# Optimization experiments

Measured on AMD Instinct MI355X. Metric: run time of the kernel, lower is better.

The kernel has to match this reference:

```python
import jax, jax.numpy as jnp
import numpy as np

N, E = 40000, 640000
IN_DIM, EDGE_DIM, HID, H1 = 5, 11, 128, 4
NEG_SLOPE = 0.2


def _add_self_loops(ei, ea, n):
    # PyG GATConv default: add_self_loops=True, fill_value='mean' for edge_attr
    loop = jnp.arange(n, dtype=ei.dtype)
    ei2 = jnp.concatenate([ei, jnp.stack([loop, loop])], axis=1)
    ea2 = jnp.concatenate([ea, jnp.broadcast_to(ea.mean(0), (n, ea.shape[1]))], axis=0)
    return ei2, ea2


def _gat(x, ei, ea, W, We, a_src, a_dst, a_edge, b, H, C):
    # Single GATConv layer (eval mode, dropout inactive)
    n = x.shape[0]
    xh = (x @ W).reshape(n, H, C)            # [N,H,C]
    eh = (ea @ We).reshape(-1, H, C)         # [E,H,C]
    src, dst = ei[0], ei[1]
    a_s = (xh * a_src).sum(-1)               # [N,H]
    a_d = (xh * a_dst).sum(-1)               # [N,H]
    alpha = jax.nn.leaky_relu(a_s[src] + a_d[dst] + (eh * a_edge).sum(-1), NEG_SLOPE)  # [E,H]
    amax = jax.ops.segment_max(alpha, dst, num_segments=n)
    ex = jnp.exp(alpha - amax[dst])
    den = jax.ops.segment_sum(ex, dst, num_segments=n)
    w = ex / (den[dst] + 1e-16)              # softmax over inbound edges per dst
    out = jax.ops.segment_sum(xh[src] * w[:, :, None], dst, num_segments=n)  # [N,H,C]
    return out.reshape(n, H * C) + b


def setup_inputs() -> dict:
    key = jax.random.key(0)
    ks = jax.random.split(key, 20)
    s = 0.1
    return {
        "x": jax.random.normal(ks[0], (N, IN_DIM), jnp.float32),
        "edge_index": jax.random.randint(ks[1], (2, E), 0, N),
        "edge_attr": jax.random.normal(ks[2], (E, EDGE_DIM), jnp.float32),
        "W1": jax.random.normal(ks[3], (IN_DIM, H1 * HID), jnp.float32) * s,
        "We1": jax.random.normal(ks[4], (EDGE_DIM, H1 * HID), jnp.float32) * s,
        "a_src1": jax.random.normal(ks[5], (H1, HID), jnp.float32) * s,
        "a_dst1": jax.random.normal(ks[6], (H1, HID), jnp.float32) * s,
        "a_edge1": jax.random.normal(ks[7], (H1, HID), jnp.float32) * s,
        "b1": jnp.zeros((H1 * HID,), jnp.float32),
        # layer 2 (512 -> 128, 1 head)
        "W2": jax.random.normal(ks[8], (H1 * HID, HID), jnp.float32) * s,
        "We2": jax.random.normal(ks[9], (EDGE_DIM, HID), jnp.float32) * s,
        "a_src2": jax.random.normal(ks[10], (1, HID), jnp.float32) * s,
        "a_dst2": jax.random.normal(ks[11], (1, HID), jnp.float32) * s,
        "a_edge2": jax.random.normal(ks[12], (1, HID), jnp.float32) * s,
        "b2": jnp.zeros((HID,), jnp.float32),
        # final linear 128 -> 1
        "Wfc": jax.random.normal(ks[13], (HID, 1), jnp.float32) * s,
        "bfc": jnp.zeros((1,), jnp.float32),
    }


def reference(x, edge_index, edge_attr,
              W1, We1, a_src1, a_dst1, a_edge1, b1,
              W2, We2, a_src2, a_dst2, a_edge2, b2,
              Wfc, bfc):
    ei, ea = _add_self_loops(edge_index, edge_attr, x.shape[0])
    h = jax.nn.relu(_gat(x, ei, ea, W1, We1, a_src1, a_dst1, a_edge1, b1, H1, HID))
    h = jax.nn.relu(_gat(h, ei, ea, W2, We2, a_src2, a_dst2, a_edge2, b2, 1, HID))
    return jax.nn.sigmoid(h @ Wfc + bfc)
```

## Files before the change

### kernel.cpp

```cpp
#include <hip/hip_runtime.h>

#define NN   40000
#define EE   640000
#define IND  5
#define ED   11
#define HIDD 128
#define F1   512
#define PSB  2500

typedef unsigned short u16;
typedef unsigned int   u32;
typedef __attribute__((ext_vector_type(8))) short bf16x8;
typedef __attribute__((ext_vector_type(4))) float f32x4;

__device__ __forceinline__ float bf2f(u16 u) { return __uint_as_float(((u32)u) << 16); }
__device__ __forceinline__ u16 f2bf(float f) {
    u32 u = __float_as_uint(f);
    return (u16)((u + 0x7FFFu + ((u >> 16) & 1u)) >> 16);
}

__device__ __forceinline__ float wsum(float v) {
#pragma unroll
    for (int o = 32; o; o >>= 1) v += __shfl_xor(v, o, 64);
    return v;
}
__device__ __forceinline__ float lrelu(float v) { return v > 0.f ? v : 0.2f * v; }


#define SBLK 256
#define SGRID ((NN + SBLK - 1) / SBLK)
#define PREPG (PSB + 33 + NN / 4)

__global__ void __launch_bounds__(256) k_prep(const int* __restrict__ ei,
                                              int* __restrict__ counts,
                                              int* __restrict__ rank,
                                              float* __restrict__ consts,
                                              const float* __restrict__ We1,
                                              const float* __restrict__ ae1,
                                              const float* __restrict__ We2,
                                              const float* __restrict__ ae2,
                                              const float* __restrict__ W2,
                                              u16* __restrict__ bsw,
                                              const float* __restrict__ x,
                                              const float* __restrict__ W1,
                                              const float* __restrict__ as1,
                                              const float* __restrict__ ad1,
                                              float* __restrict__ aS1,
                                              float* __restrict__ aD1) {
    int bid = blockIdx.x, t = threadIdx.x;
    if (bid < PSB) {
        int i = bid * 256 + t;
        rank[i] = atomicAdd(&counts[ei[EE + i]], 1);
        return;
    }
    if (bid == PSB) {
        if (t < 44) {
            int k = t >> 2, h = t & 3;
            float s = 0.f;
            for (int c = 0; c < HIDD; ++c)
                s += We1[k * F1 + h * HIDD + c] * ae1[h * HIDD + c];
            consts[16 + t] = s;
        }
        if (t >= 48 && t < 48 + ED) {
            int k = t - 48;
            float s = 0.f;
            for (int c = 0; c < HIDD; ++c)
                s += We2[k * HIDD + c] * ae2[c];
            consts[64 + k] = s;
        }
        return;
    }
    if (bid < PSB + 33) {
        int t2 = (bid - (PSB + 1)) * 256 + t;
        if (t2 >= 8192) return;
        int lane = t2 & 63, ks = (t2 >> 6) & 15, nt = t2 >> 10;
        int kbase = ks * 32 + (lane >> 4) * 8;
        int n = nt * 16 + (lane & 15);
        size_t dst = (size_t)t2 * 8;
#pragma unroll
        for (int j = 0; j < 8; ++j)
            bsw[dst + j] = f2bf(W2[(size_t)(kbase + j) * HIDD + n]);
        return;
    }
    int n = (bid - (PSB + 33)) * 4 + (t >> 6);
    int lane = t & 63;
    int c0 = lane * 8, h = lane >> 4;
    const float* xp = x + (size_t)n * IND;
    float x0 = xp[0], x1 = xp[1], x2 = xp[2], x3 = xp[3], x4 = xp[4];
    float p = 0.f, q = 0.f;
#pragma unroll
    for (int j = 0; j < 8; ++j) {
        int c = c0 + j;
        float v = x0 * W1[0 * F1 + c] + x1 * W1[1 * F1 + c] + x2 * W1[2 * F1 + c]
                + x3 * W1[3 * F1 + c] + x4 * W1[4 * F1 + c];
        p += v * as1[c];
        q += v * ad1[c];
    }
#pragma unroll
    for (int o = 1; o <= 8; o <<= 1) {
        p += __shfl_xor(p, o, 64);
        q += __shfl_xor(q, o, 64);
    }
    if ((lane & 15) == 0) {
        aS1[n * 4 + h] = p;
        aD1[n * 4 + h] = q;
    }
}

__global__ void __launch_bounds__(SBLK) k_scan(const int* __restrict__ counts,
                                               int* __restrict__ row_off) {
    __shared__ int sh[SBLK];
    __shared__ int s_boff;
    int t = threadIdx.x, b = blockIdx.x;
    int acc = 0;
    for (int i = t; i < b * SBLK; i += SBLK) acc += counts[i];
    sh[t] = acc;
    __syncthreads();
    for (int o = 128; o; o >>= 1) {
        if (t < o) sh[t] += sh[t + o];
        __syncthreads();
    }
    if (t == 0) s_boff = sh[0];
    __syncthreads();
    int boff = s_boff;
    __syncthreads();
    int i = b * SBLK + t;
    int v = (i < NN) ? counts[i] : 0;
    sh[t] = v;
    __syncthreads();
    for (int o = 1; o < SBLK; o <<= 1) {
        int u = (t >= o) ? sh[t - o] : 0;
        __syncthreads();
        sh[t] += u;
        __syncthreads();
    }
    if (i < NN) row_off[i] = boff + sh[t] - v;
    if (b == 0 && t == 0) row_off[NN] = EE;
}

__global__ void __launch_bounds__(256) k_build(const float* __restrict__ ea,
                                               const int* __restrict__ ei,
                                               const int* __restrict__ rank,
                                               const int* __restrict__ row_off,
                                               const float* __restrict__ consts,
                                               uint4* __restrict__ rec,
                                               float* __restrict__ psum) {
    __shared__ float shf[4 * ED];
    int t = threadIdx.x;
    int i = blockIdx.x * 256 + t;
    int s = ei[i];
    int d = ei[EE + i];
    int pos = row_off[d] + rank[i];
    const float* row = ea + (size_t)i * ED;
    float r[ED];
#pragma unroll
    for (int k = 0; k < ED; ++k) r[k] = row[k];
    float e0 = 0.f, e1 = 0.f, e2 = 0.f, e3 = 0.f, et = 0.f;
#pragma unroll
    for (int k = 0; k < ED; ++k) {
        float a = r[k];
        e0 += a * consts[16 + k * 4 + 0];
        e1 += a * consts[16 + k * 4 + 1];
        e2 += a * consts[16 + k * 4 + 2];
        e3 += a * consts[16 + k * 4 + 3];
        et += a * consts[64 + k];
    }
    uint4 q;
    q.x = (u32)f2bf(e0) | ((u32)f2bf(e1) << 16);
    q.y = (u32)f2bf(e2) | ((u32)f2bf(e3) << 16);
    q.z = (u32)s;
    q.w = __float_as_uint(et);
    rec[pos] = q;
#pragma unroll
    for (int k = 0; k < ED; ++k) r[k] = wsum(r[k]);
    int wv = t >> 6, lane = t & 63;
    if (lane < ED) shf[wv * ED + lane] = r[lane];
    __syncthreads();
    if (t < ED)
        psum[(size_t)blockIdx.x * ED + t] =
            shf[t] + shf[ED + t] + shf[2 * ED + t] + shf[3 * ED + t];
}

__global__ void __launch_bounds__(256) k_sumred(const float* __restrict__ psum,
                                                float* __restrict__ consts) {
    __shared__ float sh[4 * ED];
    __shared__ float mean[ED];
    int t = threadIdx.x;
    float acc[ED];
#pragma unroll
    for (int k = 0; k < ED; ++k) acc[k] = 0.f;
    for (int w = t; w < PSB; w += 256) {
        const float* p = psum + (size_t)w * ED;
#pragma unroll
        for (int k = 0; k < ED; ++k) acc[k] += p[k];
    }
#pragma unroll
    for (int k = 0; k < ED; ++k) acc[k] = wsum(acc[k]);
    int wv = t >> 6, lane = t & 63;
    if (lane < ED) sh[wv * ED + lane] = acc[lane];
    __syncthreads();
    if (t < ED) {
        float m = (sh[t] + sh[ED + t] + sh[2 * ED + t] + sh[3 * ED + t])
                  * (1.0f / (float)EE);
        mean[t] = m;
    }
    __syncthreads();
    if (t < 4) {
        float s = 0.f;
        for (int k = 0; k < ED; ++k) s += mean[k] * consts[16 + k * 4 + t];
        consts[80 + t] = s;
    }
    if (t == 8) {
        float s = 0.f;
        for (int k = 0; k < ED; ++k) s += mean[k] * consts[64 + k];
        consts[96] = s;
    }
}

__global__ void __launch_bounds__(256) k_agg1(const int* __restrict__ row_off,
                                              const uint4* __restrict__ rec,
                                              const float* __restrict__ aS1,
                                              const float* __restrict__ aD1,
                                              const float* __restrict__ x,
                                              const float* __restrict__ W1,
                                              const float* __restrict__ b1,
                                              const float* __restrict__ consts,
                                              u16* __restrict__ h1) {
    int n = blockIdx.x * 4 + (threadIdx.x >> 6);
    int t = threadIdx.x & 63;
    int s0 = row_off[n], s1 = row_off[n + 1];
    int h = t & 3;
    float4 adv = *(const float4*)(aD1 + (size_t)n * 4);
    float adh = (h == 0) ? adv.x : (h == 1) ? adv.y : (h == 2) ? adv.z : adv.w;
    float z = 0.f, xa0 = 0.f, xa1 = 0.f, xa2 = 0.f, xa3 = 0.f, xa4 = 0.f;
    for (int i = s0 + (t >> 2); i < s1; i += 16) {
        uint4 q = rec[i];
        u32 w2 = (h & 2) ? q.y : q.x;
        float eh = bf2f((h & 1) ? (u16)(w2 >> 16) : (u16)(w2 & 0xFFFF));
        int s = (int)q.z;
        float a = lrelu(eh + aS1[(size_t)s * 4 + h] + adh);
        float ex = __expf(a);
        z += ex;
        const float* xp = x + (size_t)s * IND;
        xa0 += ex * xp[0]; xa1 += ex * xp[1]; xa2 += ex * xp[2];
        xa3 += ex * xp[3]; xa4 += ex * xp[4];
    }
    if (t < 4) {
        float a = lrelu(consts[80 + h] + aS1[(size_t)n * 4 + h] + adh);
        float ex = __expf(a);
        z += ex;
        const float* xp = x + (size_t)n * IND;
        xa0 += ex * xp[0]; xa1 += ex * xp[1]; xa2 += ex * xp[2];
        xa3 += ex * xp[3]; xa4 += ex * xp[4];
    }
#pragma unroll
    for (int o = 4; o <= 32; o <<= 1) {
        z   += __shfl_xor(z, o, 64);
        xa0 += __shfl_xor(xa0, o, 64); xa1 += __shfl_xor(xa1, o, 64);
        xa2 += __shfl_xor(xa2, o, 64); xa3 += __shfl_xor(xa3, o, 64);
        xa4 += __shfl_xor(xa4, o, 64);
    }
    int ho = t >> 4;
    float zz = __shfl(z, ho);
    float y0 = __shfl(xa0, ho), y1 = __shfl(xa1, ho), y2 = __shfl(xa2, ho);
    float y3 = __shfl(xa3, ho), y4 = __shfl(xa4, ho);
    float ih = 1.f / (zz + 1e-16f);
    int c0 = t * 8;
#pragma unroll
    for (int j = 0; j < 8; ++j) {
        int c = c0 + j;
        float v = (y0 * W1[0 * F1 + c] + y1 * W1[1 * F1 + c] + y2 * W1[2 * F1 + c]
                 + y3 * W1[3 * F1 + c] + y4 * W1[4 * F1 + c]) * ih;
        h1[(size_t)n * F1 + c] = f2bf(fmaxf(v + b1[c], 0.f));
    }
}

__global__ void __launch_bounds__(256, 2) k_gemm2(const u16* __restrict__ h1,
                                                  const u16* __restrict__ bsw,
                                                  const float* __restrict__ as2,
                                                  const float* __restrict__ ad2,
                                                  u16* __restrict__ xh2,
                                                  float* __restrict__ aS2,
                                                  float* __restrict__ aD2) {
    int tid = threadIdx.x;
    int wv = tid >> 6, lane = tid & 63;
    int tile = blockIdx.x * 4 + wv;
    if (tile >= 2500) return;
    int n0 = tile * 16;
    int mrow = lane & 15, quad = lane >> 4;
    const u16* aptr = h1 + (size_t)(n0 + mrow) * F1 + quad * 8;
    const u16* bbase = bsw + lane * 8;
    f32x4 acc[8];
#pragma unroll
    for (int nt = 0; nt < 8; ++nt) acc[nt] = (f32x4){0.f, 0.f, 0.f, 0.f};

    bf16x8 b0[8], b1v[8];
    bf16x8 af0, af1;
    af0 = *(const bf16x8*)(aptr);
#pragma unroll
    for (int nt = 0; nt < 8; ++nt)
        b0[nt] = *(const bf16x8*)(bbase + nt * 8192);
#pragma unroll
    for (int ks = 0; ks < 16; ++ks) {
        if (ks < 15) {
            af1 = *(const bf16x8*)(aptr + (ks + 1) * 32);
#pragma unroll
            for (int nt = 0; nt < 8; ++nt)
                b1v[nt] = *(const bf16x8*)(bbase + nt * 8192 + (ks + 1) * 512);
        }
#pragma unroll
        for (int nt = 0; nt < 8; ++nt)
            acc[nt] = __builtin_amdgcn_mfma_f32_16x16x32_bf16(af0, b0[nt], acc[nt], 0, 0, 0);
        af0 = af1;
#pragma unroll
        for (int nt = 0; nt < 8; ++nt) b0[nt] = b1v[nt];
    }
    float ps[4] = {0.f, 0.f, 0.f, 0.f}, pd[4] = {0.f, 0.f, 0.f, 0.f};
#pragma unroll
    for (int nt = 0; nt < 8; ++nt) {
        int col = nt * 16 + mrow;
        float sa = as2[col], da = ad2[col];
#pragma unroll
        for (int r = 0; r < 4; ++r) {
            float v = acc[nt][r];
            xh2[(size_t)(n0 + quad * 4 + r) * HIDD + col] = f2bf(v);
            ps[r] += v * sa; pd[r] += v * da;
        }
    }
#pragma unroll
    for (int r = 0; r < 4; ++r) {
#pragma unroll
        for (int o = 1; o <= 8; o <<= 1) {
            ps[r] += __shfl_xor(ps[r], o, 64);
            pd[r] += __shfl_xor(pd[r], o, 64);
        }
        if (mrow == 0) {
            aS2[n0 + quad * 4 + r] = ps[r];
            aD2[n0 + quad * 4 + r] = pd[r];
        }
    }
}

__global__ void __launch_bounds__(256) k_agg2(const int* __restrict__ row_off,
                                              const uint4* __restrict__ rec,
                                              const float* __restrict__ aS2,
                                              const float* __restrict__ aD2,
                                              const u16* __restrict__ xh2,
                                              const float* __restrict__ bias2,
                                              const float* __restrict__ Wfc,
                                              const float* __restrict__ bfc,
                                              const float* __restrict__ consts,
                                              float* __restrict__ out) {
    int n = blockIdx.x * 4 + (threadIdx.x >> 6);
    int t = threadIdx.x & 63;
    int s0 = row_off[n], s1 = row_off[n + 1];
    float adn = aD2[n];
    int g = t >> 4, l = t & 15;
    int c0 = l * 8;
    float z = 0.f;
    float acc[8];
#pragma unroll
    for (int j = 0; j < 8; ++j) acc[j] = 0.f;
    for (int i = s0 + g; i < s1; i += 4) {
        uint4 qe = rec[i];
        int s = (int)qe.z;
        float et2 = __uint_as_float(qe.w);
        float ex = __expf(lrelu(aS2[s] + adn + et2));
        z += ex;
        uint4 q = *(const uint4*)(xh2 + (size_t)s * HIDD + c0);
        acc[0] += ex * bf2f((u16)(q.x & 0xFFFF)); acc[1] += ex * bf2f((u16)(q.x >> 16));
        acc[2] += ex * bf2f((u16)(q.y & 0xFFFF)); acc[3] += ex * bf2f((u16)(q.y >> 16));
        acc[4] += ex * bf2f((u16)(q.z & 0xFFFF)); acc[5] += ex * bf2f((u16)(q.z >> 16));
        acc[6] += ex * bf2f((u16)(q.w & 0xFFFF)); acc[7] += ex * bf2f((u16)(q.w >> 16));
    }
    if (g == 0) {
        float ex = __expf(lrelu(aS2[n] + adn + consts[96]));
        z += ex;
        uint4 q = *(const uint4*)(xh2 + (size_t)n * HIDD + c0);
        acc[0] += ex * bf2f((u16)(q.x & 0xFFFF)); acc[1] += ex * bf2f((u16)(q.x >> 16));
        acc[2] += ex * bf2f((u16)(q.y & 0xFFFF)); acc[3] += ex * bf2f((u16)(q.y >> 16));
        acc[4] += ex * bf2f((u16)(q.z & 0xFFFF)); acc[5] += ex * bf2f((u16)(q.z >> 16));
        acc[6] += ex * bf2f((u16)(q.w & 0xFFFF)); acc[7] += ex * bf2f((u16)(q.w >> 16));
    }
#pragma unroll
    for (int o = 16; o <= 32; o <<= 1) {
        z += __shfl_xor(z, o, 64);
#pragma unroll
        for (int j = 0; j < 8; ++j) acc[j] += __shfl_xor(acc[j], o, 64);
    }
    float inv = 1.f / (z + 1e-16f);
    float p = 0.f;
#pragma unroll
    for (int j = 0; j < 8; ++j) {
        float o = fmaxf(acc[j] * inv + bias2[c0 + j], 0.f);
        p += o * Wfc[c0 + j];
    }
#pragma unroll
    for (int o = 1; o <= 8; o <<= 1) p += __shfl_xor(p, o, 64);
    if (t == 0) {
        float logit = p + bfc[0];
        out[n] = 1.f / (1.f + __expf(-logit));
    }
}

extern "C" void kernel_launch(void* const* d_in, const int* in_sizes, int n_in,
                              void* d_out, int out_size, void* d_ws, size_t ws_size,
                              hipStream_t stream) {
    (void)in_sizes; (void)n_in; (void)out_size; (void)ws_size;
    const float* x   = (const float*)d_in[0];
    const int*   ei  = (const int*)d_in[1];
    const float* ea  = (const float*)d_in[2];
    const float* W1  = (const float*)d_in[3];
    const float* We1 = (const float*)d_in[4];
    const float* as1 = (const float*)d_in[5];
    const float* ad1 = (const float*)d_in[6];
    const float* ae1 = (const float*)d_in[7];
    const float* b1  = (const float*)d_in[8];
    const float* W2  = (const float*)d_in[9];
    const float* We2 = (const float*)d_in[10];
    const float* as2 = (const float*)d_in[11];
    const float* ad2 = (const float*)d_in[12];
    const float* ae2 = (const float*)d_in[13];
    const float* b2v = (const float*)d_in[14];
    const float* Wfc = (const float*)d_in[15];
    const float* bfc = (const float*)d_in[16];
    float* out = (float*)d_out;

    char* ws = (char*)d_ws;
    size_t off = 0;
    auto take = [&](size_t nb) {
        size_t r = off;
        off += (nb + 255) & ~(size_t)255;
        return r;
    };
    float* consts = (float*)(ws + take(1024));
    int*   counts = (int*)(ws + take((size_t)NN * 4));
    size_t zbytes = off;
    int* row_off  = (int*)(ws + take((size_t)(NN + 1) * 4));
    int* rank     = (int*)(ws + take((size_t)EE * 4));
    float* psum   = (float*)(ws + take((size_t)PSB * ED * 4));
    uint4* rec    = (uint4*)(ws + take((size_t)EE * 16));
    float* aS1    = (float*)(ws + take((size_t)NN * 16));
    float* aD1    = (float*)(ws + take((size_t)NN * 16));
    float* aS2    = (float*)(ws + take((size_t)NN * 4));
    float* aD2    = (float*)(ws + take((size_t)NN * 4));
    u16* h1       = (u16*)(ws + take((size_t)NN * F1 * 2));
    u16* xh2      = (u16*)(ws + take((size_t)NN * HIDD * 2));
    u16* w2b      = (u16*)(ws + take((size_t)65536 * 2));

    hipMemsetAsync(ws, 0, zbytes, stream);
    k_prep<<<PREPG, 256, 0, stream>>>(ei, counts, rank, consts, We1, ae1, We2, ae2,
                                      W2, w2b, x, W1, as1, ad1, aS1, aD1);
    k_scan<<<SGRID, SBLK, 0, stream>>>(counts, row_off);
    k_build<<<PSB, 256, 0, stream>>>(ea, ei, rank, row_off, consts, rec, psum);
    k_sumred<<<1, 256, 0, stream>>>(psum, consts);
    k_agg1<<<NN / 4, 256, 0, stream>>>(row_off, rec, aS1, aD1, x, W1, b1, consts, h1);
    k_gemm2<<<625, 256, 0, stream>>>(h1, w2b, as2, ad2, xh2, aS2, aD2);
    k_agg2<<<NN / 4, 256, 0, stream>>>(row_off, rec, aS2, aD2, xh2, b2v, Wfc, bfc,
                                       consts, out);
}
```

Measured before the change: 270.5 us.

## Remap agg1 to 16 lanes per node handling all heads; widen sumred to 1024 threads

k_agg1 now gives each 16-lane group of a wave one destination node, and each lane handles all four heads per edge. This replaces the old layout of 64 lanes per node with 4 lanes per head, removes the redundant per-head rec/aS1 loads, and packs h1 writes into 16-byte stores. k_sumred grows from 256 to 1024 threads to shorten its serial loop. The register-indexed shared stores are rewritten as unrolled compares so the arrays avoid scratch memory. The cost is more registers per lane for 24 accumulators and less parallelism per node on high-degree nodes.

```diff
diff --git a/kernel.cpp b/kernel.cpp
--- a/kernel.cpp
+++ b/kernel.cpp
@@ -174,22 +174,24 @@
 #pragma unroll
     for (int k = 0; k < ED; ++k) r[k] = wsum(r[k]);
     int wv = t >> 6, lane = t & 63;
-    if (lane < ED) shf[wv * ED + lane] = r[lane];
+#pragma unroll
+    for (int k = 0; k < ED; ++k)
+        if (lane == k) shf[wv * ED + k] = r[k];
     __syncthreads();
     if (t < ED)
         psum[(size_t)blockIdx.x * ED + t] =
             shf[t] + shf[ED + t] + shf[2 * ED + t] + shf[3 * ED + t];
 }
 
-__global__ void __launch_bounds__(256) k_sumred(const float* __restrict__ psum,
-                                                float* __restrict__ consts) {
-    __shared__ float sh[4 * ED];
+__global__ void __launch_bounds__(1024) k_sumred(const float* __restrict__ psum,
+                                                 float* __restrict__ consts) {
+    __shared__ float sh[16 * ED];
     __shared__ float mean[ED];
     int t = threadIdx.x;
     float acc[ED];
 #pragma unroll
     for (int k = 0; k < ED; ++k) acc[k] = 0.f;
-    for (int w = t; w < PSB; w += 256) {
+    for (int w = t; w < PSB; w += 1024) {
         const float* p = psum + (size_t)w * ED;
 #pragma unroll
         for (int k = 0; k < ED; ++k) acc[k] += p[k];
@@ -197,12 +199,15 @@
 #pragma unroll
     for (int k = 0; k < ED; ++k) acc[k] = wsum(acc[k]);
     int wv = t >> 6, lane = t & 63;
-    if (lane < ED) sh[wv * ED + lane] = acc[lane];
+#pragma unroll
+    for (int k = 0; k < ED; ++k)
+        if (lane == k) sh[wv * ED + k] = acc[k];
     __syncthreads();
     if (t < ED) {
-        float m = (sh[t] + sh[ED + t] + sh[2 * ED + t] + sh[3 * ED + t])
-                  * (1.0f / (float)EE);
-        mean[t] = m;
+        float m = 0.f;
+#pragma unroll
+        for (int v = 0; v < 16; ++v) m += sh[v * ED + t];
+        mean[t] = m * (1.0f / (float)EE);
     }
     __syncthreads();
     if (t < 4) {
@@ -226,52 +231,88 @@
                                               const float* __restrict__ b1,
                                               const float* __restrict__ consts,
                                               u16* __restrict__ h1) {
-    int n = blockIdx.x * 4 + (threadIdx.x >> 6);
-    int t = threadIdx.x & 63;
+    int wv = threadIdx.x >> 6, lane = threadIdx.x & 63;
+    int g = lane >> 4, sl = lane & 15;
+    int n = blockIdx.x * 16 + wv * 4 + g;
     int s0 = row_off[n], s1 = row_off[n + 1];
-    int h = t & 3;
     float4 adv = *(const float4*)(aD1 + (size_t)n * 4);
-    float adh = (h == 0) ? adv.x : (h == 1) ? adv.y : (h == 2) ? adv.z : adv.w;
-    float z = 0.f, xa0 = 0.f, xa1 = 0.f, xa2 = 0.f, xa3 = 0.f, xa4 = 0.f;
-    for (int i = s0 + (t >> 2); i < s1; i += 16) {
+    float z0 = 0.f, z1 = 0.f, z2 = 0.f, z3 = 0.f;
+    float xa[4][5];
+#pragma unroll
+    for (int h = 0; h < 4; ++h)
+#pragma unroll
+        for (int j = 0; j < 5; ++j) xa[h][j] = 0.f;
+
+    for (int i = s0 + sl; i < s1; i += 16) {
         uint4 q = rec[i];
-        u32 w2 = (h & 2) ? q.y : q.x;
-        float eh = bf2f((h & 1) ? (u16)(w2 >> 16) : (u16)(w2 & 0xFFFF));
         int s = (int)q.z;
-        float a = lrelu(eh + aS1[(size_t)s * 4 + h] + adh);
-        float ex = __expf(a);
-        z += ex;
+        float e0 = bf2f((u16)(q.x & 0xFFFF)), e1 = bf2f((u16)(q.x >> 16));
+        float e2 = bf2f((u16)(q.y & 0xFFFF)), e3 = bf2f((u16)(q.y >> 16));
+        float4 as4 = *(const float4*)(aS1 + (size_t)s * 4);
         const float* xp = x + (size_t)s * IND;
-        xa0 += ex * xp[0]; xa1 += ex * xp[1]; xa2 += ex * xp[2];
-        xa3 += ex * xp[3]; xa4 += ex * xp[4];
-    }
-    if (t < 4) {
-        float a = lrelu(consts[80 + h] + aS1[(size_t)n * 4 + h] + adh);
-        float ex = __expf(a);
-        z += ex;
+        float x0 = xp[0], x1 = xp[1], x2 = xp[2], x3 = xp[3], x4 = xp[4];
+        float ex;
+        ex = __expf(lrelu(e0 + as4.x + adv.x)); z0 += ex;
+        xa[0][0] += ex * x0; xa[0][1] += ex * x1; xa[0][2] += ex * x2;
+        xa[0][3] += ex * x3; xa[0][4] += ex * x4;
+        ex = __expf(lrelu(e1 + as4.y + adv.y)); z1 += ex;
+        xa[1][0] += ex * x0; xa[1][1] += ex * x1; xa[1][2] += ex * x2;
+        xa[1][3] += ex * x3; xa[1][4] += ex * x4;
+        ex = __expf(lrelu(e2 + as4.z + adv.z)); z2 += ex;
+        xa[2][0] += ex * x0; xa[2][1] += ex * x1; xa[2][2] += ex * x2;
+        xa[2][3] += ex * x3; xa[2][4] += ex * x4;
+        ex = __expf(lrelu(e3 + as4.w + adv.w)); z3 += ex;
+        xa[3][0] += ex * x0; xa[3][1] += ex * x1; xa[3][2] += ex * x2;
+        xa[3][3] += ex * x3; xa[3][4] += ex * x4;
+    }
+    if (sl == 0) {
+        float4 as4 = *(const float4*)(aS1 + (size_t)n * 4);
         const float* xp = x + (size_t)n * IND;
-        xa0 += ex * xp[0]; xa1 += ex * xp[1]; xa2 += ex * xp[2];
-        xa3 += ex * xp[3]; xa4 += ex * xp[4];
-    }
-#pragma unroll
-    for (int o = 4; o <= 32; o <<= 1) {
-        z   += __shfl_xor(z, o, 64);
-        xa0 += __shfl_xor(xa0, o, 64); xa1 += __shfl_xor(xa1, o, 64);
-        xa2 += __shfl_xor(xa2, o, 64); xa3 += __shfl_xor(xa3, o, 64);
-        xa4 += __shfl_xor(xa4, o, 64);
-    }
-    int ho = t >> 4;
-    float zz = __shfl(z, ho);
-    float y0 = __shfl(xa0, ho), y1 = __shfl(xa1, ho), y2 = __shfl(xa2, ho);
-    float y3 = __shfl(xa3, ho), y4 = __shfl(xa4, ho);
-    float ih = 1.f / (zz + 1e-16f);
-    int c0 = t * 8;
-#pragma unroll
-    for (int j = 0; j < 8; ++j) {
-        int c = c0 + j;
-        float v = (y0 * W1[0 * F1 + c] + y1 * W1[1 * F1 + c] + y2 * W1[2 * F1 + c]
-                 + y3 * W1[3 * F1 + c] + y4 * W1[4 * F1 + c]) * ih;
-        h1[(size_t)n * F1 + c] = f2bf(fmaxf(v + b1[c], 0.f));
+        float x0 = xp[0], x1 = xp[1], x2 = xp[2], x3 = xp[3], x4 = xp[4];
+        float ex;
+        ex = __expf(lrelu(consts[80] + as4.x + adv.x)); z0 += ex;
+        xa[0][0] += ex * x0; xa[0][1] += ex * x1; xa[0][2] += ex * x2;
+        xa[0][3] += ex * x3; xa[0][4] += ex * x4;
+        ex = __expf(lrelu(consts[81] + as4.y + adv.y)); z1 += ex;
+        xa[1][0] += ex * x0; xa[1][1] += ex * x1; xa[1][2] += ex * x2;
+        xa[1][3] += ex * x3; xa[1][4] += ex * x4;
+        ex = __expf(lrelu(consts[82] + as4.z + adv.z)); z2 += ex;
+        xa[2][0] += ex * x0; xa[2][1] += ex * x1; xa[2][2] += ex * x2;
+        xa[2][3] += ex * x3; xa[2][4] += ex * x4;
+        ex = __expf(lrelu(consts[83] + as4.w + adv.w)); z3 += ex;
+        xa[3][0] += ex * x0; xa[3][1] += ex * x1; xa[3][2] += ex * x2;
+        xa[3][3] += ex * x3; xa[3][4] += ex * x4;
+    }
+#pragma unroll
+    for (int o = 1; o <= 8; o <<= 1) {
+        z0 += __shfl_xor(z0, o, 64); z1 += __shfl_xor(z1, o, 64);
+        z2 += __shfl_xor(z2, o, 64); z3 += __shfl_xor(z3, o, 64);
+#pragma unroll
+        for (int h = 0; h < 4; ++h)
+#pragma unroll
+            for (int j = 0; j < 5; ++j) xa[h][j] += __shfl_xor(xa[h][j], o, 64);
+    }
+    float zz[4] = {z0, z1, z2, z3};
+#pragma unroll
+    for (int cb = 0; cb < 4; ++cb) {
+        float ih = 1.f / (zz[cb] + 1e-16f);
+        int c0 = cb * 128 + sl * 8;
+        u32 wp[4];
+#pragma unroll
+        for (int jj = 0; jj < 4; ++jj) {
+            int c = c0 + jj * 2;
+            float v0 = (xa[cb][0] * W1[0 * F1 + c] + xa[cb][1] * W1[1 * F1 + c]
+                      + xa[cb][2] * W1[2 * F1 + c] + xa[cb][3] * W1[3 * F1 + c]
+                      + xa[cb][4] * W1[4 * F1 + c]) * ih;
+            float v1 = (xa[cb][0] * W1[0 * F1 + c + 1] + xa[cb][1] * W1[1 * F1 + c + 1]
+                      + xa[cb][2] * W1[2 * F1 + c + 1] + xa[cb][3] * W1[3 * F1 + c + 1]
+                      + xa[cb][4] * W1[4 * F1 + c + 1]) * ih;
+            v0 = fmaxf(v0 + b1[c], 0.f);
+            v1 = fmaxf(v1 + b1[c + 1], 0.f);
+            wp[jj] = (u32)f2bf(v0) | ((u32)f2bf(v1) << 16);
+        }
+        uint4 st; st.x = wp[0]; st.y = wp[1]; st.z = wp[2]; st.w = wp[3];
+        *(uint4*)(h1 + (size_t)n * F1 + c0) = st;
     }
 }
 
@@ -453,8 +494,8 @@
                                       W2, w2b, x, W1, as1, ad1, aS1, aD1);
     k_scan<<<SGRID, SBLK, 0, stream>>>(counts, row_off);
     k_build<<<PSB, 256, 0, stream>>>(ea, ei, rank, row_off, consts, rec, psum);
-    k_sumred<<<1, 256, 0, stream>>>(psum, consts);
-    k_agg1<<<NN / 4, 256, 0, stream>>>(row_off, rec, aS1, aD1, x, W1, b1, consts, h1);
+    k_sumred<<<1, 1024, 0, stream>>>(psum, consts);
+    k_agg1<<<NN / 16, 256, 0, stream>>>(row_off, rec, aS1, aD1, x, W1, b1, consts, h1);
     k_gemm2<<<625, 256, 0, stream>>>(h1, w2b, as2, ad2, xh2, aS2, aD2);
     k_agg2<<<NN / 4, 256, 0, stream>>>(row_off, rec, aS2, aD2, xh2, b2v, Wfc, bfc,
                                        consts, out);
```

Result: slower. 279.2 us (+3.2%).
